# Performance work log

Hardware: AMD Instinct MI355X
Metric: run time of the kernel (lower is better)

The kernel has to match this reference:

```python
import jax, jax.numpy as jnp
import numpy as np

M_BITS = 4            # mem_pot_bits
M_MASK = (1 << M_BITS) - 1
T_MASK = (1 << 4) - 1  # t_bits = 4
ALPHA = 0.5


def setup_inputs() -> dict:
    key = jax.random.key(0)
    ks = jax.random.split(key, 8)
    B, N_IN, N_OUT, M = 256, 4096, 4096, 1 << M_BITS
    return {
        "active_mask": jax.random.randint(ks[0], (B, N_IN), 0, 2, dtype=jnp.int32),
        "t": 7,
        "prev_neuron_id": jax.random.randint(ks[1], (N_IN,), 0, M, dtype=jnp.int32),
        "t_last": jnp.zeros((B,), jnp.int32),
        "mem_fict": jax.random.uniform(ks[2], (B, N_OUT), jnp.float32),
        "mem_phys": jax.random.randint(ks[3], (B, N_OUT), 0, M, dtype=jnp.int32),
        "accumulate_lut_delta": jnp.zeros((N_OUT, M), jnp.float32),
        "tau": jax.random.uniform(ks[4], (N_OUT,), jnp.float32),
        "v_th": jax.random.uniform(ks[5], (N_OUT,), jnp.float32),
        "syn_w": jax.random.uniform(ks[6], (N_IN, N_OUT), jnp.float32),
        "mem_map": jax.nn.sigmoid(jax.random.normal(ks[7], (N_OUT, M), jnp.float32)),
    }


def reference(active_mask, t, prev_neuron_id, t_last, mem_fict, mem_phys,
              accumulate_lut_delta, tau, v_th, syn_w, mem_map):
    # delta_t = (t - t_last) & t_bit_mask  (Python '&' binds looser than '-')
    delta_t = (t - t_last) & T_MASK                          # (B,)
    t_last_new = jnp.full_like(t_last, t)

    # masked matmul + exponential membrane decay
    weights_sum = active_mask.astype(jnp.float32) @ syn_w    # (B, N_out)
    decay = jnp.exp(-tau[None, :] * delta_t[:, None].astype(jnp.float32))
    mem_fict_new = mem_fict * decay + weights_sum

    # XOR tree-reduction over masked input ids == bitwise parity per bit.
    # Only the low M_BITS matter (result is masked by m_bit_mask afterwards).
    masked_ids = jnp.where(active_mask.astype(bool), prev_neuron_id[None, :], 0)
    shifts = jnp.arange(M_BITS, dtype=jnp.int32)
    bits = (masked_ids[:, :, None] >> shifts) & 1            # (B, N_in, M_BITS)
    parity = jnp.sum(bits, axis=1) & 1                       # (B, M_BITS)
    acc = jnp.sum(parity << shifts, axis=1)                  # (B,)

    # physical membrane update (all low-bit integer ops)
    mem_phys_new = (mem_phys ^ delta_t[:, None] ^ acc[:, None]) & M_MASK

    # LUT gather + threshold
    n_out = mem_map.shape[0]
    rows = jnp.broadcast_to(jnp.arange(n_out)[None, :], mem_phys_new.shape)
    v_map_vals = mem_map[rows, mem_phys_new]                 # (B, N_out)
    active_next = v_map_vals >= v_th[None, :]

    # scatter-add per-bucket LUT delta (alpha != 0 path)
    delta = ALPHA * (mem_phys_new.astype(jnp.float32) - v_map_vals)
    lut_new = accumulate_lut_delta.at[rows, mem_phys_new].add(delta)

    return active_next, mem_fict_new, mem_phys_new, lut_new, t_last_new
```

## Files before the change

### kernel.cpp

```cpp
#include <hip/hip_runtime.h>

typedef __attribute__((ext_vector_type(8))) short short8;
typedef __attribute__((ext_vector_type(4))) float f32x4;
typedef unsigned int u32;

#define N_IN  4096
#define N_OUT 4096
#define NBAT  256

#define OUT_ACT   0
#define OUT_FICT  1048576
#define OUT_PHYS  2097152
#define OUT_LUT   3145728
#define OUT_TLAST 3211264

#define WS_MASK   0
#define WS_PART   2097152
#define WS_DTF    (WS_PART + 16777216)
#define WS_DXA    (WS_DTF + 1024)

#define BM 128
#define BN 64
#define BK 64
#define SPLITK 4
#define KCHUNK (N_IN / SPLITK)
#define NTK (KCHUNK / BK)

__device__ __forceinline__ unsigned f2bf(float f) {
  unsigned u = __float_as_uint(f);
  return (u + 0x7FFFu + ((u >> 16) & 1u)) >> 16;
}

__device__ __forceinline__ void gload16(const void* g, void* l) {
  __builtin_amdgcn_global_load_lds(
      (const __attribute__((address_space(1))) u32*)g,
      (__attribute__((address_space(3))) u32*)l, 16, 0, 0);
}

__global__ __launch_bounds__(256) void snn_pre(
    const int* __restrict__ mask, const int* __restrict__ t_ptr,
    const int* __restrict__ pid, const int* __restrict__ t_last,
    float* __restrict__ dtf_ws, int* __restrict__ dxa_ws,
    u32* __restrict__ maskws, float* __restrict__ out)
{
  const int b = blockIdx.x, tid = threadIdx.x;
  const int k0 = tid * 16;
  const int4* mp = (const int4*)(mask + (size_t)b * N_IN + k0);
  const int4* pp = (const int4*)(pid + k0);
  int x = 0;
  u32 wv[8];
#pragma unroll
  for (int q = 0; q < 4; ++q) {
    int4 m = mp[q];
    int4 id = pp[q];
    x ^= (m.x ? id.x : 0) ^ (m.y ? id.y : 0) ^ (m.z ? id.z : 0) ^ (m.w ? id.w : 0);
    wv[q * 2]     = (m.x ? 0x3F80u : 0u) | ((m.y ? 0x3F80u : 0u) << 16);
    wv[q * 2 + 1] = (m.z ? 0x3F80u : 0u) | ((m.w ? 0x3F80u : 0u) << 16);
  }
  {
    const int kt = tid >> 2;
    const int gg = (tid & 3) * 2;
    u32* base = maskws + (size_t)b * 2048 + kt * 32;
    int g0 = gg ^ (b & 7), g1 = (gg + 1) ^ (b & 7);
    uint4 v0; v0.x = wv[0]; v0.y = wv[1]; v0.z = wv[2]; v0.w = wv[3];
    uint4 v1; v1.x = wv[4]; v1.y = wv[5]; v1.z = wv[6]; v1.w = wv[7];
    *(uint4*)(base + g0 * 4) = v0;
    *(uint4*)(base + g1 * 4) = v1;
  }
  x ^= __shfl_xor(x, 32); x ^= __shfl_xor(x, 16); x ^= __shfl_xor(x, 8);
  x ^= __shfl_xor(x, 4);  x ^= __shfl_xor(x, 2);  x ^= __shfl_xor(x, 1);
  __shared__ int wx[4];
  if ((tid & 63) == 0) wx[tid >> 6] = x;
  __syncthreads();
  if (tid == 0) {
    int acc = wx[0] ^ wx[1] ^ wx[2] ^ wx[3];
    int tt = t_ptr[0];
    int dt = (tt - t_last[b]) & 15;
    dtf_ws[b] = (float)dt;
    dxa_ws[b] = dt ^ (acc & 15);
    out[OUT_TLAST + b] = (float)tt;
  }
}

__global__ __launch_bounds__(256) void snn_gemm(
    const char* __restrict__ maskws, const float* __restrict__ synw,
    float* __restrict__ part)
{
  __shared__ __align__(16) char ldsA[2][BM * BK * 2];
  __shared__ __align__(16) char ldsB[2][BN * BK * 2];

  const int tid = threadIdx.x;
  const int lane = tid & 63, wid = tid >> 6;
  const int l15 = lane & 15, l4 = lane >> 4;
  const int mb = blockIdx.x, nb = blockIdx.y, sp = blockIdx.z;
  const int bmb = mb * BM, bnb = nb * BN, kcb = sp * KCHUNK;
  const int wm = wid >> 1, wn = wid & 1;

  const char* a_gbase = maskws + (size_t)bmb * 8192 + (size_t)kcb * 2;
  const int b_n = tid & 63;
  const int b_kq = tid >> 6;
  const float* b_gbase = synw + (size_t)(kcb + b_kq * 16) * N_OUT + bnb + b_n;
  float bv[16];

  auto issueA = [&](int buf, int kt) {
#pragma unroll
    for (int i = 0; i < 4; ++i) {
      const char* g = a_gbase + (size_t)(i * 32 + (tid >> 3)) * 8192 + kt * 128 + (tid & 7) * 16;
      gload16(g, &ldsA[buf][i * 4096 + wid * 1024]);
    }
  };
  auto loadB = [&](int kt) {
    const float* g = b_gbase + (size_t)kt * BK * N_OUT;
#pragma unroll
    for (int j = 0; j < 16; ++j) bv[j] = g[(size_t)j * N_OUT];
  };
  auto writeB = [&](int buf) {
    u32 w[8];
#pragma unroll
    for (int p = 0; p < 8; ++p) w[p] = f2bf(bv[2 * p]) | (f2bf(bv[2 * p + 1]) << 16);
    const int gb = b_kq * 2, s = b_n & 7;
    uint4 v0; v0.x = w[0]; v0.y = w[1]; v0.z = w[2]; v0.w = w[3];
    uint4 v1; v1.x = w[4]; v1.y = w[5]; v1.z = w[6]; v1.w = w[7];
    *(uint4*)(&ldsB[buf][b_n * 128 + ((gb ^ s) * 16)]) = v0;
    *(uint4*)(&ldsB[buf][b_n * 128 + (((gb + 1) ^ s) * 16)]) = v1;
  };

  f32x4 acc[4][2] = {};

  auto compute = [&](int buf) {
#pragma unroll
    for (int kk = 0; kk < 2; ++kk) {
      const int g0 = kk * 4 + l4;
      short8 a[4], b[2];
#pragma unroll
      for (int mi = 0; mi < 4; ++mi) {
        int row = wm * 64 + mi * 16 + l15;
        a[mi] = *(const short8*)(&ldsA[buf][row * 128 + ((g0 ^ (row & 7)) * 16)]);
      }
#pragma unroll
      for (int nj = 0; nj < 2; ++nj) {
        int col = wn * 32 + nj * 16 + l15;
        b[nj] = *(const short8*)(&ldsB[buf][col * 128 + ((g0 ^ (col & 7)) * 16)]);
      }
#pragma unroll
      for (int mi = 0; mi < 4; ++mi)
#pragma unroll
        for (int nj = 0; nj < 2; ++nj)
          acc[mi][nj] = __builtin_amdgcn_mfma_f32_16x16x32_bf16(a[mi], b[nj], acc[mi][nj], 0, 0, 0);
    }
  };

  issueA(0, 0); loadB(0); writeB(0);
  __syncthreads();

  for (int kt = 0; kt < NTK; ++kt) {
    const int cur = kt & 1;
    if (kt + 1 < NTK) { issueA(cur ^ 1, kt + 1); loadB(kt + 1); }
    compute(cur);
    if (kt + 1 < NTK) writeB(cur ^ 1);
    __syncthreads();
  }

  float* pb = part + (size_t)sp * (NBAT * N_OUT);
#pragma unroll
  for (int mi = 0; mi < 4; ++mi)
#pragma unroll
    for (int nj = 0; nj < 2; ++nj) {
      const int o = bnb + wn * 32 + nj * 16 + l15;
#pragma unroll
      for (int r = 0; r < 4; ++r) {
        const int b = bmb + wm * 64 + mi * 16 + l4 * 4 + r;
        pb[(size_t)b * N_OUT + o] = acc[mi][nj][r];
      }
    }
}

__global__ __launch_bounds__(256) void snn_reduce(
    const float* __restrict__ part, const float* __restrict__ memf,
    const int* __restrict__ memp, const float* __restrict__ tau,
    const float* __restrict__ vth, const float* __restrict__ mem_map,
    const float* __restrict__ dtf_ws, const int* __restrict__ dxa_ws,
    float* __restrict__ out)
{
  const int flat = (blockIdx.x * 256 + threadIdx.x) * 4;
  const int b = flat >> 12, o = flat & 4095;
  const float4 p0 = *(const float4*)(part + flat);
  const float4 p1 = *(const float4*)(part + 1048576 + flat);
  const float4 p2 = *(const float4*)(part + 2097152 + flat);
  const float4 p3 = *(const float4*)(part + 3145728 + flat);
  float4 ws;
  ws.x = (p0.x + p1.x) + (p2.x + p3.x);
  ws.y = (p0.y + p1.y) + (p2.y + p3.y);
  ws.z = (p0.z + p1.z) + (p2.z + p3.z);
  ws.w = (p0.w + p1.w) + (p2.w + p3.w);
  const float dtf = dtf_ws[b];
  const int dxa = dxa_ws[b];
  const float4 mf = *(const float4*)(memf + flat);
  const int4  mp = *(const int4*)(memp + flat);
  const float4 tv = *(const float4*)(tau + o);
  const float4 vv = *(const float4*)(vth + o);
  float4 act, fict, phys;
#define DO(c, oi) { float d = __expf(-tv.c * dtf); fict.c = mf.c * d + ws.c; \
                    int mpn = (mp.c ^ dxa) & 15; phys.c = (float)mpn; \
                    act.c = (mem_map[(o + oi) * 16 + mpn] >= vv.c) ? 1.f : 0.f; }
  DO(x, 0) DO(y, 1) DO(z, 2) DO(w, 3)
#undef DO
  *(float4*)(out + OUT_ACT  + flat) = act;
  *(float4*)(out + OUT_FICT + flat) = fict;
  *(float4*)(out + OUT_PHYS + flat) = phys;
}

__global__ __launch_bounds__(256) void snn_lut(
    const int* __restrict__ memp, const int* __restrict__ dxa_ws,
    const float* __restrict__ mem_map, const float* __restrict__ lut_in,
    float* __restrict__ out)
{
  __shared__ int mp[NBAT * 16];
  __shared__ int dxs[NBAT];
  const int tid = threadIdx.x;
  const int o0 = blockIdx.x * 16;
#pragma unroll
  for (int i = 0; i < 16; ++i) {
    int b = i * 16 + (tid >> 4);
    int oj = tid & 15;
    mp[b * 16 + oj] = memp[(size_t)b * N_OUT + o0 + oj];
  }
  dxs[tid] = dxa_ws[tid];
  __syncthreads();
  const int o_l = tid >> 4, m = tid & 15;
  int cnt = 0;
#pragma unroll 8
  for (int b = 0; b < NBAT; ++b) {
    int v = (mp[b * 16 + o_l] ^ dxs[b]) & 15;
    cnt += (v == m);
  }
  const int o = o0 + o_l;
  const float vmap = mem_map[o * 16 + m];
  out[OUT_LUT + o * 16 + m] = lut_in[o * 16 + m] + 0.5f * ((float)m - vmap) * (float)cnt;
}

extern "C" void kernel_launch(void* const* d_in, const int* in_sizes, int n_in,
                              void* d_out, int out_size, void* d_ws, size_t ws_size,
                              hipStream_t stream)
{
  const int*   mask    = (const int*)d_in[0];
  const int*   t_ptr   = (const int*)d_in[1];
  const int*   pid     = (const int*)d_in[2];
  const int*   t_last  = (const int*)d_in[3];
  const float* memf    = (const float*)d_in[4];
  const int*   memp    = (const int*)d_in[5];
  const float* lut_in  = (const float*)d_in[6];
  const float* tau     = (const float*)d_in[7];
  const float* vth     = (const float*)d_in[8];
  const float* synw    = (const float*)d_in[9];
  const float* mem_map = (const float*)d_in[10];
  float* out = (float*)d_out;

  char* wsb = (char*)d_ws;
  u32*   maskws = (u32*)(wsb + WS_MASK);
  float* part   = (float*)(wsb + WS_PART);
  float* dtf_ws = (float*)(wsb + WS_DTF);
  int*   dxa_ws = (int*)(wsb + WS_DXA);

  snn_pre<<<NBAT, 256, 0, stream>>>(mask, t_ptr, pid, t_last, dtf_ws, dxa_ws, maskws, out);
  snn_gemm<<<dim3(NBAT / BM, N_OUT / BN, SPLITK), 256, 0, stream>>>(
      (const char*)maskws, synw, part);
  snn_reduce<<<(NBAT * N_OUT) / 1024, 256, 0, stream>>>(
      part, memf, memp, tau, vth, mem_map, dtf_ws, dxa_ws, out);
  snn_lut<<<NBAT, 256, 0, stream>>>(memp, dxa_ws, mem_map, lut_in, out);
}
```

Measured before the change: 52.67 us.

## Triple-buffer A tiles and double-buffer B registers with one barrier per step

The GEMM main loop is restructured. A tiles get three LDS buffers and are issued two k-steps ahead. B tiles are double-buffered in registers, and the loop is unrolled by two so each k-step has a single barrier, with explicit lgkmcnt waits and scheduling barriers. The goal is to hide global load latency and cut synchronization stalls. This costs an extra 16 KB of LDS and more live registers, relies on in-order vmcnt retirement for correctness, and assumes NTK is even.

```diff
diff --git a/kernel.cpp b/kernel.cpp
--- a/kernel.cpp
+++ b/kernel.cpp
@@ -86,35 +86,34 @@
     const char* __restrict__ maskws, const float* __restrict__ synw,
     float* __restrict__ part)
 {
-  __shared__ __align__(16) char ldsA[2][BM * BK * 2];
+  __shared__ __align__(16) char ldsA[3][BM * BK * 2];
   __shared__ __align__(16) char ldsB[2][BN * BK * 2];
 
   const int tid = threadIdx.x;
   const int lane = tid & 63, wid = tid >> 6;
   const int l15 = lane & 15, l4 = lane >> 4;
-  const int mb = blockIdx.x, nb = blockIdx.y, sp = blockIdx.z;
-  const int bmb = mb * BM, bnb = nb * BN, kcb = sp * KCHUNK;
+  const int bmb = blockIdx.x * BM, bnb = blockIdx.y * BN;
+  const int kcb = blockIdx.z * KCHUNK;
   const int wm = wid >> 1, wn = wid & 1;
 
   const char* a_gbase = maskws + (size_t)bmb * 8192 + (size_t)kcb * 2;
   const int b_n = tid & 63;
   const int b_kq = tid >> 6;
   const float* b_gbase = synw + (size_t)(kcb + b_kq * 16) * N_OUT + bnb + b_n;
-  float bv[16];
-
-  auto issueA = [&](int buf, int kt) {
-#pragma unroll
-    for (int i = 0; i < 4; ++i) {
-      const char* g = a_gbase + (size_t)(i * 32 + (tid >> 3)) * 8192 + kt * 128 + (tid & 7) * 16;
-      gload16(g, &ldsA[buf][i * 4096 + wid * 1024]);
-    }
-  };
-  auto loadB = [&](int kt) {
+
+  auto issueA = [&](int kt) {
+    char* dbase = &ldsA[kt % 3][wid * 1024];
+    const char* g0 = a_gbase + (size_t)(tid >> 3) * 8192 + kt * 128 + (tid & 7) * 16;
+#pragma unroll
+    for (int i = 0; i < 4; ++i)
+      gload16(g0 + (size_t)i * (32 * 8192), dbase + i * 4096);
+  };
+  auto loadB = [&](int kt, float* bv) {
     const float* g = b_gbase + (size_t)kt * BK * N_OUT;
 #pragma unroll
     for (int j = 0; j < 16; ++j) bv[j] = g[(size_t)j * N_OUT];
   };
-  auto writeB = [&](int buf) {
+  auto writeB = [&](const float* bv, int buf) {
     u32 w[8];
 #pragma unroll
     for (int p = 0; p < 8; ++p) w[p] = f2bf(bv[2 * p]) | (f2bf(bv[2 * p + 1]) << 16);
@@ -127,7 +126,7 @@
 
   f32x4 acc[4][2] = {};
 
-  auto compute = [&](int buf) {
+  auto compute = [&](int abuf, int bbuf) {
 #pragma unroll
     for (int kk = 0; kk < 2; ++kk) {
       const int g0 = kk * 4 + l4;
@@ -135,12 +134,12 @@
 #pragma unroll
       for (int mi = 0; mi < 4; ++mi) {
         int row = wm * 64 + mi * 16 + l15;
-        a[mi] = *(const short8*)(&ldsA[buf][row * 128 + ((g0 ^ (row & 7)) * 16)]);
+        a[mi] = *(const short8*)(&ldsA[abuf][row * 128 + ((g0 ^ (row & 7)) * 16)]);
       }
 #pragma unroll
       for (int nj = 0; nj < 2; ++nj) {
         int col = wn * 32 + nj * 16 + l15;
-        b[nj] = *(const short8*)(&ldsB[buf][col * 128 + ((g0 ^ (col & 7)) * 16)]);
+        b[nj] = *(const short8*)(&ldsB[bbuf][col * 128 + ((g0 ^ (col & 7)) * 16)]);
       }
 #pragma unroll
       for (int mi = 0; mi < 4; ++mi)
@@ -150,18 +149,31 @@
     }
   };
 
-  issueA(0, 0); loadB(0); writeB(0);
-  __syncthreads();
-
-  for (int kt = 0; kt < NTK; ++kt) {
-    const int cur = kt & 1;
-    if (kt + 1 < NTK) { issueA(cur ^ 1, kt + 1); loadB(kt + 1); }
-    compute(cur);
-    if (kt + 1 < NTK) writeB(cur ^ 1);
-    __syncthreads();
-  }
-
-  float* pb = part + (size_t)sp * (NBAT * N_OUT);
+  float bvA[16], bvB[16];
+
+  issueA(0);
+  loadB(0, bvA);
+  issueA(1);
+
+#define BODY(KT, CURBV, NXTBV)                                   \
+  {                                                              \
+    if ((KT) + 1 < NTK) loadB((KT) + 1, NXTBV);                  \
+    writeB(CURBV, (KT) & 1);  \
+    __builtin_amdgcn_sched_barrier(0);                           \
+    asm volatile("s_waitcnt lgkmcnt(0)" ::: "memory");           \
+    __builtin_amdgcn_s_barrier();                                \
+    __builtin_amdgcn_sched_barrier(0);                           \
+    if ((KT) + 2 < NTK) issueA((KT) + 2);                        \
+    compute((KT) % 3, (KT) & 1);                                 \
+  }
+
+  for (int kt = 0; kt < NTK; kt += 2) {
+    BODY(kt, bvA, bvB);
+    BODY(kt + 1, bvB, bvA);
+  }
+#undef BODY
+
+  float* pb = part + (size_t)blockIdx.z * (NBAT * N_OUT);
 #pragma unroll
   for (int mi = 0; mi < 4; ++mi)
 #pragma unroll
```

After: 50.85 us. -3.5%, faster.
